# Kernel optimization log

Measured on AMD Instinct MI355X. Metric: run time of the kernel, lower is better.

## Reference

```python
import jax, jax.numpy as jnp
import numpy as np


def setup_inputs() -> dict:
    key = jax.random.key(0)
    doc_embeddings = jax.random.normal(key, (16384, 128), dtype=jnp.float32)
    return {"doc_embeddings": doc_embeddings}


def reference(doc_embeddings) -> jnp.ndarray:
    n = doc_embeddings.shape[0]
    # [N, N] pairwise dot products
    scores = jnp.matmul(doc_embeddings, doc_embeddings.T)
    positive_scores = jnp.diagonal(scores)  # [N]
    # zero out the diagonal (matches dot - eye*dot in the torch code)
    diag_mask = jnp.eye(n, dtype=scores.dtype)
    negative_scores = scores - diag_mask * scores
    positive_loss = jax.nn.log_sigmoid(positive_scores)            # [N]
    negative_loss = jax.nn.log_sigmoid(-negative_scores).sum(axis=1)  # [N]
    loss = -(positive_loss + negative_loss).mean()
    return loss
```

## Files before the change

kernel.cpp:

```cpp
#include <hip/hip_runtime.h>
#include <hip/hip_bf16.h>


#define N_DOCS 16384
#define DIM 128
#define NTILE 128
#define NTRI (NTILE * (NTILE + 1) / 2)
#define PBLOCKS 768

typedef __attribute__((ext_vector_type(4))) float f32x4;
typedef __attribute__((ext_vector_type(8))) __bf16 bf16x8;
typedef __attribute__((ext_vector_type(2))) long longx2;

typedef const __attribute__((address_space(1))) unsigned char* gptr_t;
typedef __attribute__((address_space(3))) unsigned char* lptr_t;

#define SQRT_LOG2E 1.2011224087864498f
#define LN2F 0.6931471805599453f
#define QC0 1.33985f
#define QC1 (-0.33985f)

#if __has_builtin(__builtin_amdgcn_exp2f)
#define EXP2F(x) __builtin_amdgcn_exp2f(x)
#else
#define EXP2F(x) exp2f(x)
#endif

#define BARRIER() do { asm volatile("" ::: "memory"); \
                       __builtin_amdgcn_s_barrier();  \
                       asm volatile("" ::: "memory"); } while (0)

__device__ __forceinline__ unsigned short f2bf(float f) {
  unsigned int u = __float_as_uint(f);
  u += 0x7fffu + ((u >> 16) & 1u);
  return (unsigned short)(u >> 16);
}

#if __has_builtin(__builtin_amdgcn_cvt_pk_fp8_f32)
#define HAVE_CVT_FP8 1
#else
__device__ __forceinline__ unsigned char f2e4m3(float x) {
  unsigned int u = __float_as_uint(x);
  unsigned char sgn = (unsigned char)((u >> 31) << 7);
  float ax = fabsf(x);
  if (!(ax < 464.f)) return sgn | 0x7E;
  unsigned int ua = u & 0x7FFFFFFFu;
  int e = (int)(ua >> 23) - 127;
  if (e < -6) {
    float q = rintf(ax * 512.f);
    return sgn | (unsigned char)q;
  }
  unsigned int mant = ua & 0x7FFFFFu;
  unsigned int keep = mant >> 20;
  unsigned int rest = mant & 0xFFFFFu;
  keep += (rest > 0x80000u) || (rest == 0x80000u && (keep & 1u));
  unsigned int ee = (unsigned int)(e + 7);
  if (keep == 8u) { keep = 0u; ee++; }
  if (ee >= 16u) return sgn | 0x7E;
  return sgn | (unsigned char)((ee << 3) | keep);
}
#endif

__device__ __forceinline__ void tri_decode(int g, int& tr, int& tc) {
  int r = (int)((2 * NTILE + 1 -
                 sqrtf((float)((2 * NTILE + 1) * (2 * NTILE + 1)) - 8.0f * (float)g)) * 0.5f);
  while (r * NTILE - r * (r - 1) / 2 > g) --r;
  while ((r + 1) * NTILE - (r + 1) * r / 2 <= g) ++r;
  tr = r;
  tc = r + (g - (r * NTILE - r * (r - 1) / 2));
}

__global__ void cast_kernel(const float* __restrict__ in, unsigned char* __restrict__ out,
                            float* __restrict__ accum, unsigned int* __restrict__ counter) {
  int i = blockIdx.x * blockDim.x + threadIdx.x;
  if (i == 0) { accum[0] = 0.f; *counter = 0u; }
  int row = i >> 4, kb = i & 15;
  const float4* p = reinterpret_cast<const float4*>(in + (size_t)row * 128 + kb * 8);
  float4 a = p[0], b = p[1];
  int w0, w1;
#ifdef HAVE_CVT_FP8
  w0 = __builtin_amdgcn_cvt_pk_fp8_f32(a.x * SQRT_LOG2E, a.y * SQRT_LOG2E, 0, false);
  w0 = __builtin_amdgcn_cvt_pk_fp8_f32(a.z * SQRT_LOG2E, a.w * SQRT_LOG2E, w0, true);
  w1 = __builtin_amdgcn_cvt_pk_fp8_f32(b.x * SQRT_LOG2E, b.y * SQRT_LOG2E, 0, false);
  w1 = __builtin_amdgcn_cvt_pk_fp8_f32(b.z * SQRT_LOG2E, b.w * SQRT_LOG2E, w1, true);
#else
  w0 = (int)f2e4m3(a.x * SQRT_LOG2E) | ((int)f2e4m3(a.y * SQRT_LOG2E) << 8) |
       ((int)f2e4m3(a.z * SQRT_LOG2E) << 16) | ((int)f2e4m3(a.w * SQRT_LOG2E) << 24);
  w1 = (int)f2e4m3(b.x * SQRT_LOG2E) | ((int)f2e4m3(b.y * SQRT_LOG2E) << 8) |
       ((int)f2e4m3(b.z * SQRT_LOG2E) << 16) | ((int)f2e4m3(b.w * SQRT_LOG2E) << 24);
#endif
  int slab = row >> 7, r = row & 127, g = kb & 3, s = kb >> 2;
  int off = slab * 16384 + (g * 2 + (s >> 1)) * 2048 + r * 16 + (s & 1) * 8;
  *reinterpret_cast<int2*>(out + off) = make_int2(w0, w1);
}

__global__ __launch_bounds__(512, 6) void loss_persist(const unsigned char* __restrict__ ef8,
                                                       float* __restrict__ accum,
                                                       unsigned int* __restrict__ counter,
                                                       float* __restrict__ out) {
  __shared__ alignas(16) unsigned char Asl[16384];
  __shared__ alignas(16) unsigned char Bsl[2][16384];
  __shared__ float red[8];
  const int tid = threadIdx.x;
  const int p = blockIdx.x;
  const int g0 = (p * 43) >> 2;
  const int g1 = ((p + 1) * 43) >> 2;
  const int n = g1 - g0;

  const int wid = tid >> 6;
  const int lane = tid & 63;
  const int wm = wid >> 2, wn = wid & 3;
  const int lrow = lane & 15;
  const int kgrp = lane >> 4;

  auto stageA = [&](int t) {
    const unsigned char* s = ef8 + (size_t)t * 16384;
#pragma unroll
    for (int it = 0; it < 2; ++it) {
      int pp = (it * 512 + tid) * 16;
      __builtin_amdgcn_global_load_lds((gptr_t)(s + pp), (lptr_t)(Asl + pp), 16, 0, 0);
    }
  };
  auto stageB = [&](int t, int buf) {
    const unsigned char* s = ef8 + (size_t)t * 16384;
#pragma unroll
    for (int it = 0; it < 2; ++it) {
      int pp = (it * 512 + tid) * 16;
      __builtin_amdgcn_global_load_lds((gptr_t)(s + pp), (lptr_t)(Bsl[buf] + pp), 16, 0, 0);
    }
  };

  auto compute = [&](int buf, bool diag) -> float {
    const unsigned char* As = (const unsigned char*)Asl;
    const unsigned char* Bs = (const unsigned char*)Bsl[buf];

    f32x4 acc[4][2];
#pragma unroll
    for (int a = 0; a < 4; ++a)
#pragma unroll
      for (int c = 0; c < 2; ++c) acc[a][c] = (f32x4){0.f, 0.f, 0.f, 0.f};

#pragma unroll
    for (int ks2 = 0; ks2 < 2; ++ks2) {
      longx2 af[4], bf[2];
      const int pbase = (kgrp * 2 + ks2) * 2048;
#pragma unroll
      for (int f = 0; f < 4; ++f) {
        int ar = wm * 64 + f * 16 + lrow;
        af[f] = *reinterpret_cast<const longx2*>(As + pbase + ar * 16);
      }
#pragma unroll
      for (int f = 0; f < 2; ++f) {
        int br = wn * 32 + f * 16 + lrow;
        bf[f] = *reinterpret_cast<const longx2*>(Bs + pbase + br * 16);
      }
#pragma unroll
      for (int fm = 0; fm < 4; ++fm)
#pragma unroll
        for (int fn = 0; fn < 2; ++fn) {
          acc[fm][fn] = __builtin_amdgcn_mfma_f32_16x16x32_fp8_fp8(af[fm].x, bf[fn].x,
                                                                   acc[fm][fn], 0, 0, 0);
          acc[fm][fn] = __builtin_amdgcn_mfma_f32_16x16x32_fp8_fp8(af[fm].y, bf[fn].y,
                                                                   acc[fm][fn], 0, 0, 0);
        }
    }

    float sm = 0.f, sp = 0.f;
    if (diag) {
#pragma unroll
      for (int fm = 0; fm < 4; ++fm)
#pragma unroll
        for (int fn = 0; fn < 2; ++fn)
#pragma unroll
          for (int r = 0; r < 4; ++r) {
            float v = acc[fm][fn][r];
            int il = wm * 64 + fm * 16 + kgrp * 4 + r;
            int jl = wn * 32 + fn * 16 + lrow;
            if (il == jl) v = -v;
            sm += fmaxf(v, 0.f);
            float u = EXP2F(-fabsf(v));
            sp = fmaf(u, fmaf(u, QC1, QC0), sp);
          }
      return sm + sp;
    } else {
#pragma unroll
      for (int fm = 0; fm < 4; ++fm)
#pragma unroll
        for (int fn = 0; fn < 2; ++fn)
#pragma unroll
          for (int r = 0; r < 4; ++r) {
            float v = acc[fm][fn][r];
            sm += fmaxf(v, 0.f);
            float u = EXP2F(-fabsf(v));
            sp = fmaf(u, fmaf(u, QC1, QC0), sp);
          }
      return 2.f * (sm + sp);
    }
  };

  int tr, tc;
  tri_decode(g0, tr, tc);
  float total = 0.f;
  int buf = 0;
  stageA(tr);
  stageB(tc, 0);
  for (int i = 0; i < n; ++i) {
    int ntr = tr, ntc = tc + 1;
    if (ntc == NTILE) { ntr = tr + 1; ntc = ntr; }
    const bool have_next = (i + 1 < n);
    const bool samerow = have_next && (ntr == tr);
    if (samerow) {
      stageB(ntc, buf ^ 1);
      asm volatile("s_waitcnt vmcnt(2)" ::: "memory");
    } else {
      asm volatile("s_waitcnt vmcnt(0)" ::: "memory");
    }
    BARRIER();
    total += compute(buf, tr == tc);
    BARRIER();
    if (have_next && !samerow) {
      stageA(ntr);
      stageB(ntc, buf ^ 1);
    }
    tr = ntr; tc = ntc; buf ^= 1;
  }

#pragma unroll
  for (int off = 32; off > 0; off >>= 1) total += __shfl_down(total, off);
  if (lane == 0) red[wid] = total;
  __syncthreads();
  if (tid == 0) {
    float t = red[0] + red[1] + red[2] + red[3] + red[4] + red[5] + red[6] + red[7];
    atomicAdd(accum, t);
    __threadfence();
    unsigned int old = atomicAdd(counter, 1u);
    if (old == (unsigned int)(PBLOCKS - 1)) {
      float v = atomicAdd(accum, 0.f);
      out[0] = LN2F * (v * (1.0f / (float)N_DOCS) + 1.0f);
    }
  }
}

__global__ __launch_bounds__(512, 2) void loss_fallback(const float* __restrict__ src,
                                                        float* __restrict__ accum) {
  const int b = blockIdx.x;
  int tr, tc;
  tri_decode(b, tr, tc);

  __shared__ alignas(16) unsigned short As[128 * 128];
  __shared__ alignas(16) unsigned short Bs[128 * 128];
  __shared__ float red[8];
  const int tid = threadIdx.x;

  const float4* srcA4 = (const float4*)(src + (size_t)tr * 16384);
  const float4* srcB4 = (const float4*)(src + (size_t)tc * 16384);
#pragma unroll
  for (int it = 0; it < 8; ++it) {
    int idx = it * 512 + tid;
    int L = idx * 8;
    int swz = L ^ (((L >> 8) & 7) << 4);
    float4 a = srcA4[idx];
    ushort4 oa = {f2bf(a.x * SQRT_LOG2E), f2bf(a.y * SQRT_LOG2E),
                  f2bf(a.z * SQRT_LOG2E), f2bf(a.w * SQRT_LOG2E)};
    *reinterpret_cast<ushort4*>((unsigned char*)As + swz) = oa;
    float4 bb = srcB4[idx];
    ushort4 ob = {f2bf(bb.x * SQRT_LOG2E), f2bf(bb.y * SQRT_LOG2E),
                  f2bf(bb.z * SQRT_LOG2E), f2bf(bb.w * SQRT_LOG2E)};
    *reinterpret_cast<ushort4*>((unsigned char*)Bs + swz) = ob;
  }
  __syncthreads();

  const int wid = tid >> 6;
  const int lane = tid & 63;
  const int wm = wid >> 2, wn = wid & 3;
  const int lrow = lane & 15;
  const int kgrp = lane >> 4;

  f32x4 acc[4][2];
#pragma unroll
  for (int a = 0; a < 4; ++a)
#pragma unroll
    for (int c = 0; c < 2; ++c) acc[a][c] = (f32x4){0.f, 0.f, 0.f, 0.f};

#pragma unroll
  for (int ks = 0; ks < 4; ++ks) {
    bf16x8 af[4], bfr[2];
#pragma unroll
    for (int f = 0; f < 4; ++f) {
      int ar = wm * 64 + f * 16 + lrow;
      int ab = (ar * 256 + ks * 64 + kgrp * 16) ^ ((ar & 7) << 4);
      af[f] = *reinterpret_cast<const bf16x8*>((const unsigned char*)As + ab);
    }
#pragma unroll
    for (int f = 0; f < 2; ++f) {
      int br = wn * 32 + f * 16 + lrow;
      int bb = (br * 256 + ks * 64 + kgrp * 16) ^ ((br & 7) << 4);
      bfr[f] = *reinterpret_cast<const bf16x8*>((const unsigned char*)Bs + bb);
    }
#pragma unroll
    for (int fm = 0; fm < 4; ++fm)
#pragma unroll
      for (int fn = 0; fn < 2; ++fn)
        acc[fm][fn] = __builtin_amdgcn_mfma_f32_16x16x32_bf16(af[fm], bfr[fn], acc[fm][fn], 0, 0, 0);
  }

  float sm = 0.f, sp = 0.f;
  if (tr == tc) {
#pragma unroll
    for (int fm = 0; fm < 4; ++fm)
#pragma unroll
      for (int fn = 0; fn < 2; ++fn)
#pragma unroll
        for (int r = 0; r < 4; ++r) {
          float v = acc[fm][fn][r];
          int il = wm * 64 + fm * 16 + kgrp * 4 + r;
          int jl = wn * 32 + fn * 16 + lrow;
          if (il == jl) v = -v;
          sm += fmaxf(v, 0.f);
          float u = EXP2F(-fabsf(v));
          sp = fmaf(u, fmaf(u, QC1, QC0), sp);
        }
  } else {
#pragma unroll
    for (int fm = 0; fm < 4; ++fm)
#pragma unroll
      for (int fn = 0; fn < 2; ++fn)
#pragma unroll
        for (int r = 0; r < 4; ++r) {
          float v = acc[fm][fn][r];
          sm += fmaxf(v, 0.f);
          float u = EXP2F(-fabsf(v));
          sp = fmaf(u, fmaf(u, QC1, QC0), sp);
        }
    sm *= 2.f;
    sp *= 2.f;
  }

  float lsum = sm + sp;
#pragma unroll
  for (int off = 32; off > 0; off >>= 1) lsum += __shfl_down(lsum, off);
  if (lane == 0) red[wid] = lsum;
  __syncthreads();
  if (tid == 0) {
    float t = red[0] + red[1] + red[2] + red[3] + red[4] + red[5] + red[6] + red[7];
    atomicAdd(accum, t);
  }
}

__global__ void finalize_kernel(const float* __restrict__ accum, float* __restrict__ out) {
  out[0] = LN2F * (accum[0] * (1.0f / (float)N_DOCS) + 1.0f);
}

extern "C" void kernel_launch(void* const* d_in, const int* in_sizes, int n_in,
                              void* d_out, int out_size, void* d_ws, size_t ws_size,
                              hipStream_t stream) {
  const float* E = (const float*)d_in[0];
  float* out = (float*)d_out;
  float* accum = (float*)d_ws;
  unsigned int* counter = (unsigned int*)((char*)d_ws + 64);

  const size_t need = 256 + (size_t)N_DOCS * DIM;
  if (ws_size >= need) {
    unsigned char* ef8 = (unsigned char*)d_ws + 256;
    cast_kernel<<<(N_DOCS * (DIM / 8)) / 256, 256, 0, stream>>>(E, ef8, accum, counter);
    loss_persist<<<PBLOCKS, 512, 0, stream>>>(ef8, accum, counter, out);
  } else {
    (void)hipMemsetAsync(accum, 0, sizeof(float), stream);
    loss_fallback<<<NTRI, 512, 0, stream>>>(E, accum);
    finalize_kernel<<<1, 1, 0, stream>>>(accum, out);
  }
}
```

Measured before the change: 107.8 us.

## Use softplus symmetry to replace max term with abs plus closed-form linear sums

Rewrites softplus(v) as 0.5*v + 0.5*|v| + log1p(exp(-|v|)), so the per-element epilogue only needs |v| and the diagonal special case disappears. The linear term sum of all pairwise dots is computed analytically from column sums and squared row norms in the cast kernel, then combined by the last block. The cast kernel is restructured to 128 blocks that also produce these partial sums, and the accumulators are zeroed with a memset. This trims per-element ALU work in the hot loop, but adds a memset launch and makes the cast kernel less parallel, and the linear term uses unquantized values while the abs term uses fp8 products.

```diff
diff --git a/kernel.cpp b/kernel.cpp
--- a/kernel.cpp
+++ b/kernel.cpp
@@ -70,37 +70,71 @@
   tc = r + (g - (r * NTILE - r * (r - 1) / 2));
 }
 
-__global__ void cast_kernel(const float* __restrict__ in, unsigned char* __restrict__ out,
-                            float* __restrict__ accum, unsigned int* __restrict__ counter) {
-  int i = blockIdx.x * blockDim.x + threadIdx.x;
-  if (i == 0) { accum[0] = 0.f; *counter = 0u; }
-  int row = i >> 4, kb = i & 15;
-  const float4* p = reinterpret_cast<const float4*>(in + (size_t)row * 128 + kb * 8);
-  float4 a = p[0], b = p[1];
-  int w0, w1;
+__global__ __launch_bounds__(256) void cast_kernel(const float* __restrict__ in,
+                                                   unsigned char* __restrict__ out,
+                                                   float* __restrict__ rpart,
+                                                   float* __restrict__ colpart) {
+  __shared__ float cs[16][136];
+  __shared__ float redr[4];
+  const int b = blockIdx.x, tid = threadIdx.x;
+  const int kb = tid & 15, rg = tid >> 4;
+
+  float csum[8] = {0.f, 0.f, 0.f, 0.f, 0.f, 0.f, 0.f, 0.f};
+  float rsum = 0.f;
+#pragma unroll
+  for (int it = 0; it < 8; ++it) {
+    int r = it * 16 + rg;
+    int row = b * 128 + r;
+    const float4* p = reinterpret_cast<const float4*>(in + (size_t)row * 128 + kb * 8);
+    float4 a = p[0], c = p[1];
+    float v0 = a.x * SQRT_LOG2E, v1 = a.y * SQRT_LOG2E, v2 = a.z * SQRT_LOG2E,
+          v3 = a.w * SQRT_LOG2E, v4 = c.x * SQRT_LOG2E, v5 = c.y * SQRT_LOG2E,
+          v6 = c.z * SQRT_LOG2E, v7 = c.w * SQRT_LOG2E;
+    int w0, w1;
 #ifdef HAVE_CVT_FP8
-  w0 = __builtin_amdgcn_cvt_pk_fp8_f32(a.x * SQRT_LOG2E, a.y * SQRT_LOG2E, 0, false);
-  w0 = __builtin_amdgcn_cvt_pk_fp8_f32(a.z * SQRT_LOG2E, a.w * SQRT_LOG2E, w0, true);
-  w1 = __builtin_amdgcn_cvt_pk_fp8_f32(b.x * SQRT_LOG2E, b.y * SQRT_LOG2E, 0, false);
-  w1 = __builtin_amdgcn_cvt_pk_fp8_f32(b.z * SQRT_LOG2E, b.w * SQRT_LOG2E, w1, true);
+    w0 = __builtin_amdgcn_cvt_pk_fp8_f32(v0, v1, 0, false);
+    w0 = __builtin_amdgcn_cvt_pk_fp8_f32(v2, v3, w0, true);
+    w1 = __builtin_amdgcn_cvt_pk_fp8_f32(v4, v5, 0, false);
+    w1 = __builtin_amdgcn_cvt_pk_fp8_f32(v6, v7, w1, true);
 #else
-  w0 = (int)f2e4m3(a.x * SQRT_LOG2E) | ((int)f2e4m3(a.y * SQRT_LOG2E) << 8) |
-       ((int)f2e4m3(a.z * SQRT_LOG2E) << 16) | ((int)f2e4m3(a.w * SQRT_LOG2E) << 24);
-  w1 = (int)f2e4m3(b.x * SQRT_LOG2E) | ((int)f2e4m3(b.y * SQRT_LOG2E) << 8) |
-       ((int)f2e4m3(b.z * SQRT_LOG2E) << 16) | ((int)f2e4m3(b.w * SQRT_LOG2E) << 24);
+    w0 = (int)f2e4m3(v0) | ((int)f2e4m3(v1) << 8) | ((int)f2e4m3(v2) << 16) | ((int)f2e4m3(v3) << 24);
+    w1 = (int)f2e4m3(v4) | ((int)f2e4m3(v5) << 8) | ((int)f2e4m3(v6) << 16) | ((int)f2e4m3(v7) << 24);
 #endif
-  int slab = row >> 7, r = row & 127, g = kb & 3, s = kb >> 2;
-  int off = slab * 16384 + (g * 2 + (s >> 1)) * 2048 + r * 16 + (s & 1) * 8;
-  *reinterpret_cast<int2*>(out + off) = make_int2(w0, w1);
+    int g = kb & 3, s = kb >> 2;
+    int off = b * 16384 + (g * 2 + (s >> 1)) * 2048 + r * 16 + (s & 1) * 8;
+    *reinterpret_cast<int2*>(out + off) = make_int2(w0, w1);
+    csum[0] += v0; csum[1] += v1; csum[2] += v2; csum[3] += v3;
+    csum[4] += v4; csum[5] += v5; csum[6] += v6; csum[7] += v7;
+    rsum = fmaf(v0, v0, rsum); rsum = fmaf(v1, v1, rsum);
+    rsum = fmaf(v2, v2, rsum); rsum = fmaf(v3, v3, rsum);
+    rsum = fmaf(v4, v4, rsum); rsum = fmaf(v5, v5, rsum);
+    rsum = fmaf(v6, v6, rsum); rsum = fmaf(v7, v7, rsum);
+  }
+#pragma unroll
+  for (int j = 0; j < 8; ++j) cs[rg][kb * 8 + j] = csum[j];
+#pragma unroll
+  for (int off = 32; off > 0; off >>= 1) rsum += __shfl_down(rsum, off);
+  if ((tid & 63) == 0) redr[tid >> 6] = rsum;
+  __syncthreads();
+  if (tid < 128) {
+    float s = 0.f;
+#pragma unroll
+    for (int r = 0; r < 16; ++r) s += cs[r][tid];
+    colpart[b * 128 + tid] = s;
+  }
+  if (tid == 0) rpart[b] = redr[0] + redr[1] + redr[2] + redr[3];
 }
 
 __global__ __launch_bounds__(512, 6) void loss_persist(const unsigned char* __restrict__ ef8,
                                                        float* __restrict__ accum,
                                                        unsigned int* __restrict__ counter,
+                                                       const float* __restrict__ rpart,
+                                                       const float* __restrict__ colpart,
                                                        float* __restrict__ out) {
   __shared__ alignas(16) unsigned char Asl[16384];
   __shared__ alignas(16) unsigned char Bsl[2][16384];
   __shared__ float red[8];
+  __shared__ int lastFlag;
   const int tid = threadIdx.x;
   const int p = blockIdx.x;
   const int g0 = (p * 43) >> 2;
@@ -130,7 +164,7 @@
     }
   };
 
-  auto compute = [&](int buf, bool diag) -> float {
+  auto compute = [&](int buf) -> float {
     const unsigned char* As = (const unsigned char*)Asl;
     const unsigned char* Bs = (const unsigned char*)Bsl[buf];
 
@@ -165,37 +199,19 @@
         }
     }
 
-    float sm = 0.f, sp = 0.f;
-    if (diag) {
-#pragma unroll
-      for (int fm = 0; fm < 4; ++fm)
-#pragma unroll
-        for (int fn = 0; fn < 2; ++fn)
-#pragma unroll
-          for (int r = 0; r < 4; ++r) {
-            float v = acc[fm][fn][r];
-            int il = wm * 64 + fm * 16 + kgrp * 4 + r;
-            int jl = wn * 32 + fn * 16 + lrow;
-            if (il == jl) v = -v;
-            sm += fmaxf(v, 0.f);
-            float u = EXP2F(-fabsf(v));
-            sp = fmaf(u, fmaf(u, QC1, QC0), sp);
-          }
-      return sm + sp;
-    } else {
-#pragma unroll
-      for (int fm = 0; fm < 4; ++fm)
-#pragma unroll
-        for (int fn = 0; fn < 2; ++fn)
-#pragma unroll
-          for (int r = 0; r < 4; ++r) {
-            float v = acc[fm][fn][r];
-            sm += fmaxf(v, 0.f);
-            float u = EXP2F(-fabsf(v));
-            sp = fmaf(u, fmaf(u, QC1, QC0), sp);
-          }
-      return 2.f * (sm + sp);
-    }
+    float sa = 0.f, su = 0.f;
+#pragma unroll
+    for (int fm = 0; fm < 4; ++fm)
+#pragma unroll
+      for (int fn = 0; fn < 2; ++fn)
+#pragma unroll
+        for (int r = 0; r < 4; ++r) {
+          float a = fabsf(acc[fm][fn][r]);
+          sa += a;
+          float u = EXP2F(-a);
+          su = fmaf(u, fmaf(u, QC1, QC0), su);
+        }
+    return fmaf(0.5f, sa, su);
   };
 
   int tr, tc;
@@ -216,7 +232,7 @@
       asm volatile("s_waitcnt vmcnt(0)" ::: "memory");
     }
     BARRIER();
-    total += compute(buf, tr == tc);
+    total += (tr == tc ? 1.f : 2.f) * compute(buf);
     BARRIER();
     if (have_next && !samerow) {
       stageA(ntr);
@@ -234,9 +250,27 @@
     atomicAdd(accum, t);
     __threadfence();
     unsigned int old = atomicAdd(counter, 1u);
-    if (old == (unsigned int)(PBLOCKS - 1)) {
-      float v = atomicAdd(accum, 0.f);
-      out[0] = LN2F * (v * (1.0f / (float)N_DOCS) + 1.0f);
+    lastFlag = (old == (unsigned int)(PBLOCKS - 1));
+  }
+  __syncthreads();
+  if (lastFlag) {
+    float part = 0.f;
+    if (tid < 128) {
+      float cs = 0.f;
+#pragma unroll 8
+      for (int b = 0; b < 128; ++b) cs += colpart[b * 128 + tid];
+      part = fmaf(0.5f * cs, cs, -rpart[tid]);
+    }
+    if (tid < 128) {
+#pragma unroll
+      for (int off = 32; off > 0; off >>= 1) part += __shfl_down(part, off);
+      if (lane == 0) red[wid] = part;
+    }
+    __syncthreads();
+    if (tid == 0) {
+      float tail = red[0] + red[1];
+      float acc = atomicAdd(accum, 0.f);
+      out[0] = LN2F * ((acc + tail) * (1.0f / (float)N_DOCS) + 1.0f);
     }
   }
 }
@@ -358,12 +392,15 @@
   float* out = (float*)d_out;
   float* accum = (float*)d_ws;
   unsigned int* counter = (unsigned int*)((char*)d_ws + 64);
-
-  const size_t need = 256 + (size_t)N_DOCS * DIM;
+  float* rpart = (float*)((char*)d_ws + 256);
+  float* colpart = (float*)((char*)d_ws + 1024);
+  unsigned char* ef8 = (unsigned char*)d_ws + 66560;
+
+  const size_t need = 66560 + (size_t)N_DOCS * DIM + 256;
   if (ws_size >= need) {
-    unsigned char* ef8 = (unsigned char*)d_ws + 256;
-    cast_kernel<<<(N_DOCS * (DIM / 8)) / 256, 256, 0, stream>>>(E, ef8, accum, counter);
-    loss_persist<<<PBLOCKS, 512, 0, stream>>>(ef8, accum, counter, out);
+    (void)hipMemsetAsync(d_ws, 0, 256, stream);
+    cast_kernel<<<128, 256, 0, stream>>>(E, ef8, rpart, colpart);
+    loss_persist<<<PBLOCKS, 512, 0, stream>>>(ef8, accum, counter, rpart, colpart, out);
   } else {
     (void)hipMemsetAsync(accum, 0, sizeof(float), stream);
     loss_fallback<<<NTRI, 512, 0, stream>>>(E, accum);
```

Result: no change. 106.0 us (-1.6%).
